# Kernel tuning notes

Hardware: AMD Instinct MI355X
Metric: run time of the kernel (lower is better)

## Reference

```python
import math
import jax, jax.numpy as jnp
import numpy as np

NSAMPLE = 16
HEADS = 4
ATTN = 256
EPS = 1e-5


def setup_inputs() -> dict:
    key = jax.random.key(0)
    ks = jax.random.split(key, 16)
    B, N, M, C = 2, 4096, 4096, 128

    def w(k, shape):
        return jax.random.normal(k, shape, jnp.float32) / np.sqrt(shape[-1]).astype(np.float32)

    return dict(
        pos1=jax.random.normal(ks[0], (B, 3, N), jnp.float32),
        pos2=jax.random.normal(ks[1], (B, 3, M), jnp.float32),
        feature1=jax.random.normal(ks[2], (B, C, N), jnp.float32),
        feature2=jax.random.normal(ks[3], (B, C, M), jnp.float32),
        w0=w(ks[4], (128, 2 * C + 3)), g0=jnp.ones(128), b0=jnp.zeros(128),
        w1=w(ks[5], (128, 128)), g1=jnp.ones(128), b1=jnp.zeros(128),
        w2=w(ks[6], (256, 128)), g2=jnp.ones(256), b2=jnp.zeros(256),
        qw=w(ks[7], (ATTN, 512)), qb=jnp.zeros(ATTN),
        kw=w(ks[8], (ATTN, C)), kb=jnp.zeros(ATTN),
        vw=w(ks[9], (ATTN, C)), vb=jnp.zeros(ATTN),
        ow=w(ks[10], (512, ATTN)), ob=jnp.zeros(512),
        lng=jnp.ones(512), lnb=jnp.zeros(512),
        fw=w(ks[11], (256, 512)), fb=jnp.zeros(256),
    )


def _knn_idx(p1t, p2t, k):
    # p1t: (B,N,3) queries; p2t: (B,M,3) keys. k nearest in pos2 for each pos1 point.
    d = (jnp.sum(p1t * p1t, -1, keepdims=True)
         - 2.0 * jnp.einsum('bnd,bmd->bnm', p1t, p2t)
         + jnp.sum(p2t * p2t, -1)[:, None, :])
    _, idx = jax.lax.top_k(-d, k)  # (B,N,k)
    return idx


def reference(pos1, pos2, feature1, feature2,
              w0, g0, b0, w1, g1, b1, w2, g2, b2,
              qw, qb, kw, kb, vw, vb, ow, ob, lng, lnb, fw, fb):
    B, _, N = pos1.shape
    M = pos2.shape[2]
    p1t = pos1.transpose(0, 2, 1)  # (B,N,3)
    p2t = pos2.transpose(0, 2, 1)  # (B,M,3)
    idx = _knn_idx(p1t, p2t, NSAMPLE)  # (B,N,k)

    gather = jax.vmap(lambda f, i: f[i])  # (M,C),(N,k)->(N,k,C)
    pos_diff = gather(p2t, idx) - p1t[:, :, None, :]              # (B,N,k,3)
    f2g = gather(feature2.transpose(0, 2, 1), idx)                # (B,N,k,C)
    f1r = jnp.broadcast_to(feature1.transpose(0, 2, 1)[:, :, None, :], f2g.shape)
    x = jnp.concatenate([pos_diff, f2g, f1r], -1)                 # (B,N,k,2C+3)

    # 1x1 conv + BatchNorm (training-mode batch stats, biased var) + ReLU
    for w, g, b in ((w0, g0, b0), (w1, g1, b1), (w2, g2, b2)):
        x = jnp.einsum('bnkc,oc->bnko', x, w)
        mu = x.mean((0, 1, 2))
        var = x.var((0, 1, 2))
        x = jax.nn.relu((x - mu) * jax.lax.rsqrt(var + EPS) * g + b)

    feat = jnp.concatenate([x.max(2), x.mean(2)], -1)  # (B,N,2*mlp[-1])

    hd = ATTN // HEADS
    f2t = feature2.transpose(0, 2, 1)  # (B,M,C)
    Q = (feat @ qw.T + qb).reshape(B, N, HEADS, hd).transpose(0, 2, 1, 3)
    K = (f2t @ kw.T + kb).reshape(B, M, HEADS, hd).transpose(0, 2, 1, 3)
    V = (f2t @ vw.T + vb).reshape(B, M, HEADS, hd).transpose(0, 2, 1, 3)
    attn = jax.nn.softmax(jnp.einsum('bhnd,bhmd->bhnm', Q, K) / math.sqrt(hd), axis=-1)
    o = jnp.einsum('bhnm,bhmd->bhnd', attn, V).transpose(0, 2, 1, 3).reshape(B, N, ATTN)
    o = o @ ow.T + ob

    y = feat + o
    mu = y.mean(-1, keepdims=True)
    var = y.var(-1, keepdims=True)
    y = (y - mu) * jax.lax.rsqrt(var + EPS) * lng + lnb
    y = y @ fw.T + fb                      # (B,N,mlp[-1])
    return (pos1, y.transpose(0, 2, 1))    # (B,3,N), (B,mlp[-1],N)
```

## Files before the change

kernel.cpp:

```cpp
#include <hip/hip_runtime.h>
#include <hip/hip_bf16.h>

constexpr int B_ = 2, N_ = 4096, M_ = 4096, C_ = 128;

typedef __attribute__((ext_vector_type(8))) __bf16 bf16x8;
typedef __attribute__((ext_vector_type(4))) float f32x4;

__global__ __launch_bounds__(256) void knn_part_kernel(const float* __restrict__ pos1,
                                                       const float* __restrict__ pos2,
                                                       float* __restrict__ pd,
                                                       int* __restrict__ pi) {
  __shared__ float tX[256], tY[256], tZ[256], tS[256];
  int tid = threadIdx.x;
  int bn = blockIdx.x * 256 + tid;
  int b = bn >> 12, n = bn & 4095;
  int seg = blockIdx.y;
  const float* p1 = pos1 + (long)b * 3 * N_;
  float qx = p1[n], qy = p1[N_ + n], qz = p1[2 * N_ + n];
  float s1 = __fadd_rn(__fadd_rn(__fmul_rn(qx, qx), __fmul_rn(qy, qy)), __fmul_rn(qz, qz));
  const float* p2 = pos2 + (long)b * 3 * M_ + seg * 256;
  {
    float x = p2[tid], y = p2[M_ + tid], z = p2[2 * M_ + tid];
    tX[tid] = x; tY[tid] = y; tZ[tid] = z;
    tS[tid] = __fadd_rn(__fadd_rn(__fmul_rn(x, x), __fmul_rn(y, y)), __fmul_rn(z, z));
  }
  __syncthreads();
  float rd[16]; int ri[16];
#pragma unroll
  for (int k = 0; k < 16; k++) { rd[k] = 3.0e38f; ri[k] = 0; }
  for (int mm = 0; mm < 256; mm += 8) {
    float dv[8];
#pragma unroll
    for (int u = 0; u < 8; u++) {
      float e = __fmaf_rn(qz, tZ[mm + u],
                          __fmaf_rn(qy, tY[mm + u], __fmul_rn(qx, tX[mm + u])));
      dv[u] = __fadd_rn(__fsub_rn(s1, __fadd_rn(e, e)), tS[mm + u]);
    }
    float thr = rd[15];
    bool any = false;
#pragma unroll
    for (int u = 0; u < 8; u++) any = any || (dv[u] < thr);
    if (any) {
#pragma unroll
      for (int u = 0; u < 8; u++) {
        float d = dv[u];
        if (d < rd[15]) {
          float cd = d; int ci = seg * 256 + mm + u;
#pragma unroll
          for (int k = 0; k < 16; k++) {
            bool lt = cd < rd[k];
            float td = lt ? rd[k] : cd;
            int ti = lt ? ri[k] : ci;
            rd[k] = lt ? cd : rd[k];
            ri[k] = lt ? ci : ri[k];
            cd = td; ci = ti;
          }
        }
      }
    }
  }
  long base = (long)seg * 16 * 8192 + bn;
#pragma unroll
  for (int k = 0; k < 16; k++) {
    pd[base + (long)k * 8192] = rd[k];
    pi[base + (long)k * 8192] = ri[k];
  }
}

__global__ __launch_bounds__(256) void knn_merge_kernel(const float* __restrict__ pd,
                                                        const int* __restrict__ pi,
                                                        int* __restrict__ idx) {
  int bn = blockIdx.x * 256 + threadIdx.x;
  float rd[16]; int ri[16];
#pragma unroll
  for (int k = 0; k < 16; k++) { rd[k] = 3.0e38f; ri[k] = 0; }
  for (int seg = 0; seg < 16; seg++) {
    for (int k = 0; k < 16; k++) {
      float d = pd[((long)seg * 16 + k) * 8192 + bn];
      if (d >= rd[15]) break;
      int ci = pi[((long)seg * 16 + k) * 8192 + bn];
      float cd = d;
#pragma unroll
      for (int j = 0; j < 16; j++) {
        bool lt = cd < rd[j];
        float td = lt ? rd[j] : cd;
        int ti = lt ? ri[j] : ci;
        rd[j] = lt ? cd : rd[j];
        ri[j] = lt ? ci : ri[j];
        cd = td; ci = ti;
      }
    }
  }
#pragma unroll
  for (int k = 0; k < 16; k++) idx[(long)bn * 16 + k] = ri[k];
}

__global__ __launch_bounds__(128) void g131_kernel(const float* __restrict__ pos,
                                                   const float* __restrict__ feat,
                                                   const float* __restrict__ w0,
                                                   float* __restrict__ out,
                                                   float sign, int woff) {
  __shared__ float Xs[131 * 16];
  int tid = threadIdx.x;
  long b = blockIdx.x >> 8;
  int i0 = (blockIdx.x & 255) * 16;
  for (int e = tid; e < 131 * 16; e += 128) {
    int r = e & 15, c = e >> 4;
    float v = (c < 3) ? sign * pos[b * 3 * N_ + (long)c * N_ + i0 + r]
                      : feat[b * C_ * N_ + (long)(c - 3) * N_ + i0 + r];
    Xs[c * 16 + r] = v;
  }
  __syncthreads();
  int o = tid;
  float acc[16];
#pragma unroll
  for (int r = 0; r < 16; r++) acc[r] = 0.f;
  for (int c = 0; c < 131; c++) {
    float wv = w0[(long)o * 259 + (c < 3 ? c : (woff + c - 3))];
    const float* xr = &Xs[c * 16];
#pragma unroll
    for (int r = 0; r < 16; r++) acc[r] = fmaf(xr[r], wv, acc[r]);
  }
#pragma unroll
  for (int r = 0; r < 16; r++) out[((b << 12) + i0 + r) * 128 + o] = acc[r];
}

__global__ __launch_bounds__(256) void z0stats_kernel(const int* __restrict__ idx,
                                                      const float* __restrict__ A1,
                                                      const float* __restrict__ A2,
                                                      double* __restrict__ st) {
  int tid = threadIdx.x;
  int o = tid & 127, half = tid >> 7;
  float sum = 0.f, sq = 0.f;
  int g0 = blockIdx.x * 32;
  for (int gi = 0; gi < 32; gi++) {
    int bn = g0 + gi;
    long b = bn >> 12;
    float a1 = A1[(long)bn * 128 + o];
    for (int k = half; k < 16; k += 2) {
      int m = idx[bn * 16 + k];
      float v = A2[(b * 4096 + m) * 128 + o] + a1;
      sum += v;
      sq += v * v;
    }
  }
  __shared__ float ls[256], lq[256];
  ls[tid] = sum; lq[tid] = sq;
  __syncthreads();
  if (tid < 128) {
    atomicAdd(&st[o], (double)(ls[tid] + ls[tid + 128]));
    atomicAdd(&st[128 + o], (double)(lq[tid] + lq[tid + 128]));
  }
}

__global__ __launch_bounds__(256) void statsb_kernel(const __hip_bfloat16* __restrict__ Z,
                                                     long nrows, double* __restrict__ st) {
  int tid = threadIdx.x;
  int c = tid & 127, sub = tid >> 7;
  long slot = (long)blockIdx.x * 2 + sub;
  long stride = (long)gridDim.x * 2;
  float sum = 0.f, sq = 0.f;
  for (long r = slot; r < nrows; r += stride) {
    float v = __bfloat162float(Z[r * 128 + c]);
    sum += v;
    sq += v * v;
  }
  __shared__ float ls[256], lq[256];
  ls[tid] = sum; lq[tid] = sq;
  __syncthreads();
  if (tid < 128) {
    atomicAdd(&st[c], (double)(ls[tid] + ls[tid + 128]));
    atomicAdd(&st[128 + c], (double)(lq[tid] + lq[tid + 128]));
  }
}

__global__ void bnfin_kernel(const double* __restrict__ st, const float* __restrict__ g,
                             const float* __restrict__ bb, float* __restrict__ sc,
                             float* __restrict__ sh, int CO, double inv) {
  int c = threadIdx.x;
  if (c < CO) {
    double mu = st[c] * inv;
    double var = st[CO + c] * inv - mu * mu;
    double rstd = 1.0 / sqrt(var + 1e-5);
    double scv = (double)g[c] * rstd;
    sc[c] = (float)scv;
    sh[c] = (float)((double)bb[c] - mu * scv);
  }
}

__global__ __launch_bounds__(256) void gemm1_mfma_kernel(
    const float* __restrict__ A2, const float* __restrict__ A1,
    const int* __restrict__ idxp, const float* __restrict__ w1,
    const float* __restrict__ sc0, const float* __restrict__ sh0,
    __hip_bfloat16* __restrict__ z1b) {
  __shared__ unsigned short As[64 * 136];
  __shared__ unsigned short Bs[64 * 136];
  __shared__ float scs[128], shs[128];
  int tid = threadIdx.x;
  int lane = tid & 63, w = tid >> 6;
  int cb = blockIdx.x;
  long r0 = (long)blockIdx.y * 64;
  int c0 = cb * 64;
  if (tid < 128) { scs[tid] = sc0[tid]; shs[tid] = sh0[tid]; }
  __syncthreads();
  {
    int row = tid >> 2, kb = (tid & 3) * 32;
    long g = r0 + row;
    int m = idxp[g];
    const float* a2p = &A2[(((g >> 16) << 12) + m) * 128 + kb];
    const float* a1p = &A1[(g >> 4) * 128 + kb];
    unsigned short* ap = &As[row * 136 + kb];
    const float* wp = &w1[(long)(c0 + row) * 128 + kb];
    unsigned short* bp = &Bs[row * 136 + kb];
#pragma unroll
    for (int h = 0; h < 4; h++) {
      union { unsigned short u[8]; uint4 v; } oa, ob;
#pragma unroll
      for (int j = 0; j < 8; j++) {
        int k = kb + h * 8 + j;
        float raw = a2p[h * 8 + j] + a1p[h * 8 + j];
        float v = fmaxf(0.f, fmaf(raw, scs[k], shs[k]));
        oa.u[j] = __bfloat16_as_ushort(__float2bfloat16(v));
        ob.u[j] = __bfloat16_as_ushort(__float2bfloat16(wp[h * 8 + j]));
      }
      *reinterpret_cast<uint4*>(ap + h * 8) = oa.v;
      *reinterpret_cast<uint4*>(bp + h * 8) = ob.v;
    }
  }
  __syncthreads();

  int fr = lane & 15, fk = (lane >> 4) * 8;
  bf16x8 a[4];
#pragma unroll
  for (int kk = 0; kk < 4; kk++)
    a[kk] = *reinterpret_cast<const bf16x8*>(&As[(w * 16 + fr) * 136 + kk * 32 + fk]);
  f32x4 acc[4];
#pragma unroll
  for (int n2 = 0; n2 < 4; n2++) {
    acc[n2] = (f32x4){0.f, 0.f, 0.f, 0.f};
#pragma unroll
    for (int kk = 0; kk < 4; kk++) {
      bf16x8 bfrag = *reinterpret_cast<const bf16x8*>(&Bs[(n2 * 16 + fr) * 136 + kk * 32 + fk]);
      acc[n2] = __builtin_amdgcn_mfma_f32_16x16x32_bf16(a[kk], bfrag, acc[n2], 0, 0, 0);
    }
  }
#pragma unroll
  for (int n2 = 0; n2 < 4; n2++) {
#pragma unroll
    for (int r = 0; r < 4; r++) {
      long row = r0 + w * 16 + (lane >> 4) * 4 + r;
      z1b[row * 128 + c0 + n2 * 16 + fr] = __float2bfloat16(acc[n2][r]);
    }
  }
}

template <int EPI>
__global__ __launch_bounds__(256) void gemm2_mfma_kernel(
    const __hip_bfloat16* __restrict__ z1b, const float* __restrict__ w2,
    const float* __restrict__ sc1, const float* __restrict__ sh1,
    const float* __restrict__ sc2, const float* __restrict__ sh2,
    float* __restrict__ feat, double* __restrict__ st) {
  __shared__ unsigned short As[64 * 136];
  __shared__ unsigned short Bs[64 * 136];
  __shared__ float scs[128], shs[128];
  __shared__ float Sred[4 * 64], Qred[4 * 64];
  int tid = threadIdx.x;
  int lane = tid & 63, w = tid >> 6;
  int cb = blockIdx.x;
  long r0 = (long)blockIdx.y * 64;
  int c0 = cb * 64;
  if (tid < 128) { scs[tid] = sc1[tid]; shs[tid] = sh1[tid]; }
  __syncthreads();
  {
    int row = tid >> 2, kb = (tid & 3) * 32;
    const __hip_bfloat16* zp = &z1b[(r0 + row) * 128 + kb];
    unsigned short* ap = &As[row * 136 + kb];
    const float* wp = &w2[(long)(c0 + row) * 128 + kb];
    unsigned short* bp = &Bs[row * 136 + kb];
#pragma unroll
    for (int h = 0; h < 4; h++) {
      union { unsigned short u[8]; uint4 v; } in, oa, ob;
      in.v = *reinterpret_cast<const uint4*>(zp + h * 8);
#pragma unroll
      for (int j = 0; j < 8; j++) {
        int k = kb + h * 8 + j;
        float f = __bfloat162float(__ushort_as_bfloat16(in.u[j]));
        float v = fmaxf(0.f, fmaf(f, scs[k], shs[k]));
        oa.u[j] = __bfloat16_as_ushort(__float2bfloat16(v));
        ob.u[j] = __bfloat16_as_ushort(__float2bfloat16(wp[h * 8 + j]));
      }
      *reinterpret_cast<uint4*>(ap + h * 8) = oa.v;
      *reinterpret_cast<uint4*>(bp + h * 8) = ob.v;
    }
  }
  __syncthreads();

  int fr = lane & 15, fk = (lane >> 4) * 8;
  bf16x8 a[4];
#pragma unroll
  for (int kk = 0; kk < 4; kk++)
    a[kk] = *reinterpret_cast<const bf16x8*>(&As[(w * 16 + fr) * 136 + kk * 32 + fk]);
  f32x4 acc[4];
#pragma unroll
  for (int n2 = 0; n2 < 4; n2++) {
    acc[n2] = (f32x4){0.f, 0.f, 0.f, 0.f};
#pragma unroll
    for (int kk = 0; kk < 4; kk++) {
      bf16x8 bfrag = *reinterpret_cast<const bf16x8*>(&Bs[(n2 * 16 + fr) * 136 + kk * 32 + fk]);
      acc[n2] = __builtin_amdgcn_mfma_f32_16x16x32_bf16(a[kk], bfrag, acc[n2], 0, 0, 0);
    }
  }

  if (EPI == 4) {
#pragma unroll
    for (int n2 = 0; n2 < 4; n2++) {
      float s = 0.f, q = 0.f;
#pragma unroll
      for (int r = 0; r < 4; r++) { s += acc[n2][r]; q += acc[n2][r] * acc[n2][r]; }
      s += __shfl_xor(s, 16); s += __shfl_xor(s, 32);
      q += __shfl_xor(q, 16); q += __shfl_xor(q, 32);
      if (lane < 16) { Sred[w * 64 + n2 * 16 + fr] = s; Qred[w * 64 + n2 * 16 + fr] = q; }
    }
    __syncthreads();
    if (tid < 64) {
      float S = Sred[tid] + Sred[64 + tid] + Sred[128 + tid] + Sred[192 + tid];
      float Q = Qred[tid] + Qred[64 + tid] + Qred[128 + tid] + Qred[192 + tid];
      atomicAdd(&st[c0 + tid], (double)S);
      atomicAdd(&st[256 + c0 + tid], (double)Q);
    }
  } else {
    int bn = (int)(r0 >> 4) + w;
#pragma unroll
    for (int n2 = 0; n2 < 4; n2++) {
      int c = c0 + n2 * 16 + fr;
      float scv = sc2[c], shv = sh2[c];
      float mx = -1e30f, sm = 0.f;
#pragma unroll
      for (int r = 0; r < 4; r++) {
        float v = fmaxf(0.f, fmaf(acc[n2][r], scv, shv));
        mx = fmaxf(mx, v);
        sm += v;
      }
      mx = fmaxf(mx, __shfl_xor(mx, 16)); mx = fmaxf(mx, __shfl_xor(mx, 32));
      sm += __shfl_xor(sm, 16); sm += __shfl_xor(sm, 32);
      if (lane < 16) {
        feat[(long)bn * 512 + c] = mx;
        feat[(long)bn * 512 + 256 + c] = sm * (1.f / 16.f);
      }
    }
  }
}

template <int EPI, int XM, bool BN>
__global__ __launch_bounds__(256) void gemm_kernel(
    const void* __restrict__ Xv, const float* __restrict__ W, float* __restrict__ out,
    int K, int CO, const float* __restrict__ bias, const float* __restrict__ sc,
    const float* __restrict__ sh, const float* __restrict__ res,
    __hip_bfloat16* __restrict__ obf, const float* __restrict__ A1,
    const int* __restrict__ idxp, double* __restrict__ st) {
  __shared__ float S[2][32 * 68];
  int tid = threadIdx.x;
  int tx = tid & 15, ty = tid >> 4;
  int cb = blockIdx.x;
  long r0 = (long)blockIdx.y * 64;
  int c0 = cb * 64;
  float acc[4][4];
#pragma unroll
  for (int i = 0; i < 4; i++)
#pragma unroll
    for (int j = 0; j < 4; j++) acc[i][j] = 0.f;

  for (int k0 = 0; k0 < K; k0 += 32) {
    if (XM != 1) {
      int c = tid & 31, rr = tid >> 5;
      float scv = 0.f, shv = 0.f;
      if (BN) { scv = sc[k0 + c]; shv = sh[k0 + c]; }
#pragma unroll
      for (int i = 0; i < 8; i++) {
        int r = rr + i * 8;
        long g = r0 + r;
        float v = ((const float*)Xv)[g * K + k0 + c];
        if (BN) v = fmaxf(0.f, fmaf(v, scv, shv));
        S[0][c * 68 + r] = v;
      }
    } else {
      int m = tid & 63, cc = tid >> 6;
      long b = r0 >> 12;
      long mg = (r0 & 4095) + m;
#pragma unroll
      for (int i = 0; i < 8; i++) {
        int c = cc + i * 4;
        S[0][c * 68 + m] = ((const float*)Xv)[(b * K + k0 + c) * 4096 + mg];
      }
    }
    {
      int c = tid & 31, oo = tid >> 5;
#pragma unroll
      for (int i = 0; i < 8; i++) {
        int o = oo + i * 8;
        S[1][c * 68 + o] = W[(long)(c0 + o) * K + k0 + c];
      }
    }
    __syncthreads();
#pragma unroll
    for (int kk = 0; kk < 32; kk++) {
      float4 a = *reinterpret_cast<const float4*>(&S[0][kk * 68 + ty * 4]);
      float4 bv = *reinterpret_cast<const float4*>(&S[1][kk * 68 + tx * 4]);
      float av[4] = {a.x, a.y, a.z, a.w};
      float bw[4] = {bv.x, bv.y, bv.z, bv.w};
#pragma unroll
      for (int i = 0; i < 4; i++)
#pragma unroll
        for (int j = 0; j < 4; j++) acc[i][j] = fmaf(av[i], bw[j], acc[i][j]);
    }
    __syncthreads();
  }

  if (EPI == 2) {
    const float4 b4 = *reinterpret_cast<const float4*>(&bias[c0 + tx * 4]);
#pragma unroll
    for (int i = 0; i < 4; i++) {
      long r = r0 + ty * 4 + i;
      float4 f4 = *reinterpret_cast<const float4*>(&res[r * CO + c0 + tx * 4]);
      float4 o4 = make_float4(acc[i][0] + b4.x + f4.x, acc[i][1] + b4.y + f4.y,
                              acc[i][2] + b4.z + f4.z, acc[i][3] + b4.w + f4.w);
      *reinterpret_cast<float4*>(&out[r * CO + c0 + tx * 4]) = o4;
    }
  } else if (EPI == 3) {
    float* Sf = &S[0][0];
#pragma unroll
    for (int j = 0; j < 4; j++) {
      float bj = bias[c0 + tx * 4 + j];
      float4 colv = make_float4(acc[0][j] + bj, acc[1][j] + bj, acc[2][j] + bj,
                                acc[3][j] + bj);
      *reinterpret_cast<float4*>(&Sf[(tx * 4 + j) * 68 + ty * 4]) = colv;
    }
    __syncthreads();
    long b = r0 >> 12;
    long n0 = (r0 & 4095);
    int n = tid & 63, oo = tid >> 6;
#pragma unroll
    for (int i = 0; i < 16; i++) {
      int o = oo + i * 4;
      out[(b * CO + c0 + o) * 4096L + n0 + n] = Sf[o * 68 + n];
    }
  } else if (EPI == 7) {
    long b = r0 >> 12;
    long nn = (r0 & 4095) + ty * 4;
    const float4 b4 = *reinterpret_cast<const float4*>(&bias[c0 + tx * 4]);
    __hip_bfloat16* Ob = obf + ((b * (CO >> 6) + cb) * 4096L) * 64;
#pragma unroll
    for (int i = 0; i < 4; i++) {
      union { unsigned short u[4]; uint2 v; } pk;
      pk.u[0] = __bfloat16_as_ushort(__float2bfloat16(acc[i][0] + b4.x));
      pk.u[1] = __bfloat16_as_ushort(__float2bfloat16(acc[i][1] + b4.y));
      pk.u[2] = __bfloat16_as_ushort(__float2bfloat16(acc[i][2] + b4.z));
      pk.u[3] = __bfloat16_as_ushort(__float2bfloat16(acc[i][3] + b4.w));
      *reinterpret_cast<uint2*>(&Ob[(nn + i) * 64 + tx * 4]) = pk.v;
    }
  } else if (EPI == 8) {
    float* Sf = &S[0][0];
#pragma unroll
    for (int j = 0; j < 4; j++) {
      float bj = bias[c0 + tx * 4 + j];
      float4 colv = make_float4(acc[0][j] + bj, acc[1][j] + bj, acc[2][j] + bj,
                                acc[3][j] + bj);
      *reinterpret_cast<float4*>(&Sf[(tx * 4 + j) * 68 + ty * 4]) = colv;
    }
    __syncthreads();
    long b = r0 >> 12;
    long n0 = (r0 & 4095);
    int n = tid & 63, oo = tid >> 6;
#pragma unroll
    for (int i = 0; i < 16; i++) {
      int o = oo + i * 4;
      obf[((b * 4 + cb) * 64 + o) * 4096L + n0 + n] = __float2bfloat16(Sf[o * 68 + n]);
    }
  }
}

__global__ __launch_bounds__(256) void flash_mfma_kernel(
    const __hip_bfloat16* __restrict__ Q, const __hip_bfloat16* __restrict__ Kb,
    const __hip_bfloat16* __restrict__ Vtg, float* __restrict__ O) {
  __shared__ unsigned short Ks[64 * 72];
  __shared__ unsigned short Vt[64 * 72];
  __shared__ unsigned short Ps[4][16 * 72];
  int tid = threadIdx.x;
  int lane = tid & 63, w = tid >> 6;
  int bh = blockIdx.x >> 6;
  int qt = blockIdx.x & 63;
  long base = (long)bh * 4096 * 64;
  int row0 = qt * 64 + w * 16;
  int fr = lane & 15;
  int fk = (lane >> 4) * 8;

  bf16x8 aq[2];
#pragma unroll
  for (int kk = 0; kk < 2; kk++)
    aq[kk] = *reinterpret_cast<const bf16x8*>(&Q[base + (long)(row0 + fr) * 64 + kk * 32 + fk]);

  f32x4 o[4];
#pragma unroll
  for (int i = 0; i < 4; i++) o[i] = (f32x4){0.f, 0.f, 0.f, 0.f};
  float m_run[4], l_run[4];
#pragma unroll
  for (int r = 0; r < 4; r++) { m_run[r] = -3.0e38f; l_run[r] = 0.f; }

  int skey = tid >> 2, sdc = (tid & 3) * 16;
  int vd = tid & 63, vkg = tid >> 6;
  int vsw = (vd ^ (vd >> 3)) & 7;

  for (int m0 = 0; m0 < 4096; m0 += 64) {
    __syncthreads();
    {
      const __hip_bfloat16* kp = &Kb[base + (long)(m0 + skey) * 64 + sdc];
      *reinterpret_cast<uint4*>(&Ks[skey * 72 + sdc]) =
          *reinterpret_cast<const uint4*>(kp);
      *reinterpret_cast<uint4*>(&Ks[skey * 72 + sdc + 8]) =
          *reinterpret_cast<const uint4*>(kp + 8);
#pragma unroll
      for (int j8 = 0; j8 < 2; j8++) {
        int k0 = vkg * 16 + j8 * 8;
        int kb = k0 >> 3;
        *reinterpret_cast<uint4*>(&Vt[vd * 72 + ((kb ^ vsw) << 3)]) =
            *reinterpret_cast<const uint4*>(&Vtg[base + (long)vd * 4096 + m0 + k0]);
      }
    }
    __syncthreads();

    f32x4 s[4];
#pragma unroll
    for (int n = 0; n < 4; n++) {
      s[n] = (f32x4){0.f, 0.f, 0.f, 0.f};
#pragma unroll
      for (int kk = 0; kk < 2; kk++) {
        bf16x8 bk = *reinterpret_cast<const bf16x8*>(&Ks[(n * 16 + fr) * 72 + kk * 32 + fk]);
        s[n] = __builtin_amdgcn_mfma_f32_16x16x32_bf16(aq[kk], bk, s[n], 0, 0, 0);
      }
    }

    float p[4][4];
#pragma unroll
    for (int r = 0; r < 4; r++) {
      float sv0 = s[0][r] * 0.125f, sv1 = s[1][r] * 0.125f;
      float sv2 = s[2][r] * 0.125f, sv3 = s[3][r] * 0.125f;
      float mx = fmaxf(fmaxf(sv0, sv1), fmaxf(sv2, sv3));
      mx = fmaxf(mx, __shfl_xor(mx, 1));
      mx = fmaxf(mx, __shfl_xor(mx, 2));
      mx = fmaxf(mx, __shfl_xor(mx, 4));
      mx = fmaxf(mx, __shfl_xor(mx, 8));
      float mn = fmaxf(m_run[r], mx);
      float fac = __expf(m_run[r] - mn);
      p[0][r] = __expf(sv0 - mn);
      p[1][r] = __expf(sv1 - mn);
      p[2][r] = __expf(sv2 - mn);
      p[3][r] = __expf(sv3 - mn);
      float rs = (p[0][r] + p[1][r]) + (p[2][r] + p[3][r]);
      rs += __shfl_xor(rs, 1);
      rs += __shfl_xor(rs, 2);
      rs += __shfl_xor(rs, 4);
      rs += __shfl_xor(rs, 8);
      l_run[r] = l_run[r] * fac + rs;
      m_run[r] = mn;
#pragma unroll
      for (int n2 = 0; n2 < 4; n2++) o[n2][r] *= fac;
    }

    unsigned short* pw = &Ps[w][0];
#pragma unroll
    for (int r = 0; r < 4; r++) {
      int prow = (lane >> 4) * 4 + r;
#pragma unroll
      for (int n = 0; n < 4; n++)
        pw[prow * 72 + n * 16 + fr] = __bfloat16_as_ushort(__float2bfloat16(p[n][r]));
    }
    bf16x8 ap[2];
#pragma unroll
    for (int kk = 0; kk < 2; kk++)
      ap[kk] = *reinterpret_cast<const bf16x8*>(&pw[fr * 72 + kk * 32 + fk]);

#pragma unroll
    for (int n2 = 0; n2 < 4; n2++) {
      int d = n2 * 16 + fr;
      int dsw = (d ^ (d >> 3)) & 7;
#pragma unroll
      for (int kk = 0; kk < 2; kk++) {
        int kb = kk * 4 + (lane >> 4);
        bf16x8 bv = *reinterpret_cast<const bf16x8*>(&Vt[d * 72 + ((kb ^ dsw) << 3)]);
        o[n2] = __builtin_amdgcn_mfma_f32_16x16x32_bf16(ap[kk], bv, o[n2], 0, 0, 0);
      }
    }
  }

  int b = bh >> 2, h = bh & 3;
#pragma unroll
  for (int r = 0; r < 4; r++) {
    float inv = 1.f / l_run[r];
    long nrow = (long)(b * 4096 + qt * 64 + w * 16 + (lane >> 4) * 4 + r);
#pragma unroll
    for (int n2 = 0; n2 < 4; n2++) {
      O[nrow * 256 + h * 64 + n2 * 16 + fr] = o[n2][r] * inv;
    }
  }
}

__global__ __launch_bounds__(256) void ln_kernel(float* __restrict__ y,
                                                 const float* __restrict__ lng,
                                                 const float* __restrict__ lnb) {
  long r = blockIdx.x;
  int tid = threadIdx.x;
  float v0 = y[r * 512 + tid];
  float v1 = y[r * 512 + 256 + tid];
  float s = v0 + v1;
  float q = v0 * v0 + v1 * v1;
#pragma unroll
  for (int off = 1; off < 64; off <<= 1) {
    s += __shfl_xor(s, off);
    q += __shfl_xor(q, off);
  }
  __shared__ float red[8];
  __shared__ float mv[2];
  int w = tid >> 6;
  if ((tid & 63) == 0) { red[w] = s; red[4 + w] = q; }
  __syncthreads();
  if (tid == 0) {
    float S = red[0] + red[1] + red[2] + red[3];
    float Q2 = red[4] + red[5] + red[6] + red[7];
    float mu = S * (1.f / 512.f);
    float var = Q2 * (1.f / 512.f) - mu * mu;
    mv[0] = mu;
    mv[1] = rsqrtf(var + 1e-5f);
  }
  __syncthreads();
  float mu = mv[0], rstd = mv[1];
  y[r * 512 + tid] = (v0 - mu) * rstd * lng[tid] + lnb[tid];
  y[r * 512 + 256 + tid] = (v1 - mu) * rstd * lng[256 + tid] + lnb[256 + tid];
}

__global__ void poscopy_kernel(const float* __restrict__ p, float* __restrict__ o) {
  int i = blockIdx.x * 256 + threadIdx.x;
  o[i] = p[i];
}

extern "C" void kernel_launch(void* const* d_in, const int* in_sizes, int n_in,
                              void* d_out, int out_size, void* d_ws, size_t ws_size,
                              hipStream_t stream) {
  (void)in_sizes; (void)n_in; (void)out_size; (void)ws_size;
  const float* pos1 = (const float*)d_in[0];
  const float* pos2 = (const float*)d_in[1];
  const float* f1 = (const float*)d_in[2];
  const float* f2 = (const float*)d_in[3];
  const float* w0 = (const float*)d_in[4];
  const float* g0 = (const float*)d_in[5];
  const float* b0 = (const float*)d_in[6];
  const float* w1 = (const float*)d_in[7];
  const float* g1 = (const float*)d_in[8];
  const float* b1 = (const float*)d_in[9];
  const float* w2 = (const float*)d_in[10];
  const float* g2 = (const float*)d_in[11];
  const float* b2 = (const float*)d_in[12];
  const float* qw = (const float*)d_in[13];
  const float* qb = (const float*)d_in[14];
  const float* kw = (const float*)d_in[15];
  const float* kb = (const float*)d_in[16];
  const float* vw = (const float*)d_in[17];
  const float* vb = (const float*)d_in[18];
  const float* ow = (const float*)d_in[19];
  const float* obv = (const float*)d_in[20];
  const float* lng = (const float*)d_in[21];
  const float* lnb = (const float*)d_in[22];
  const float* fw = (const float*)d_in[23];
  const float* fb = (const float*)d_in[24];

  char* ws = (char*)d_ws;
  __hip_bfloat16* z1b = (__hip_bfloat16*)(ws);
  __hip_bfloat16* Qbf = (__hip_bfloat16*)(ws);
  __hip_bfloat16* Kbf = (__hip_bfloat16*)(ws + (8ull << 20));
  __hip_bfloat16* Vtg = (__hip_bfloat16*)(ws + (16ull << 20));
  float* attno = (float*)(ws + (24ull << 20));
  float* y0 = (float*)(ws);
  int* idx = (int*)(ws + (32ull << 20));
  float* A1 = (float*)(ws + (33ull << 20));
  float* A2 = (float*)(ws + (37ull << 20));
  float* feat = (float*)(ws + (32ull << 20));
  char* statp = ws + (48ull << 20);
  float* pd = (float*)(ws + (56ull << 20));
  int* pi = (int*)(ws + (64ull << 20));
  double* st0 = (double*)(statp);
  double* st1 = (double*)(statp + 2048);
  double* st2 = (double*)(statp + 4096);
  float* sc0 = (float*)(statp + 8192);
  float* sh0 = (float*)(statp + 8704);
  float* sc1 = (float*)(statp + 9216);
  float* sh1 = (float*)(statp + 9728);
  float* sc2 = (float*)(statp + 10240);
  float* sh2 = (float*)(statp + 11264);

  float* out0 = (float*)d_out;
  float* out1 = out0 + 24576;

  hipMemsetAsync(statp, 0, 8192, stream);

  knn_part_kernel<<<dim3(32, 16), 256, 0, stream>>>(pos1, pos2, pd, pi);
  knn_merge_kernel<<<32, 256, 0, stream>>>(pd, pi, idx);
  g131_kernel<<<512, 128, 0, stream>>>(pos2, f2, w0, A2, 1.f, 3);
  g131_kernel<<<512, 128, 0, stream>>>(pos1, f1, w0, A1, -1.f, 131);
  z0stats_kernel<<<256, 256, 0, stream>>>(idx, A1, A2, st0);
  bnfin_kernel<<<1, 256, 0, stream>>>(st0, g0, b0, sc0, sh0, 128, 1.0 / 131072.0);
  gemm1_mfma_kernel<<<dim3(2, 2048), 256, 0, stream>>>(
      A2, A1, idx, w1, sc0, sh0, z1b);
  statsb_kernel<<<512, 256, 0, stream>>>(z1b, 131072L, st1);
  bnfin_kernel<<<1, 256, 0, stream>>>(st1, g1, b1, sc1, sh1, 128, 1.0 / 131072.0);
  gemm2_mfma_kernel<4><<<dim3(4, 2048), 256, 0, stream>>>(
      z1b, w2, sc1, sh1, nullptr, nullptr, nullptr, st2);
  bnfin_kernel<<<1, 256, 0, stream>>>(st2, g2, b2, sc2, sh2, 256, 1.0 / 131072.0);
  gemm2_mfma_kernel<5><<<dim3(4, 2048), 256, 0, stream>>>(
      z1b, w2, sc1, sh1, sc2, sh2, feat, nullptr);
  gemm_kernel<7, 0, false><<<dim3(4, 128), 256, 0, stream>>>(
      feat, qw, nullptr, 512, 256, qb, nullptr, nullptr, nullptr, Qbf, nullptr, nullptr, nullptr);
  gemm_kernel<7, 1, false><<<dim3(4, 128), 256, 0, stream>>>(
      f2, kw, nullptr, 128, 256, kb, nullptr, nullptr, nullptr, Kbf, nullptr, nullptr, nullptr);
  gemm_kernel<8, 1, false><<<dim3(4, 128), 256, 0, stream>>>(
      f2, vw, nullptr, 128, 256, vb, nullptr, nullptr, nullptr, Vtg, nullptr, nullptr, nullptr);
  flash_mfma_kernel<<<512, 256, 0, stream>>>(Qbf, Kbf, Vtg, attno);
  gemm_kernel<2, 0, false><<<dim3(8, 128), 256, 0, stream>>>(
      attno, ow, y0, 256, 512, obv, nullptr, nullptr, feat, nullptr, nullptr, nullptr, nullptr);
  ln_kernel<<<8192, 256, 0, stream>>>(y0, lng, lnb);
  gemm_kernel<3, 0, false><<<dim3(4, 128), 256, 0, stream>>>(
      y0, fw, out1, 512, 256, fb, nullptr, nullptr, nullptr, nullptr, nullptr, nullptr, nullptr);
  poscopy_kernel<<<96, 256, 0, stream>>>(pos1, out0);
}
```

Measured before the change: 804.6 us.

## Split flash attention over two key halves and merge partial softmax results

The flash attention kernel's grid gains a second dimension, and each block now handles only half of the 4096 keys. Each block writes a normalized partial output plus its running max and sum per row. A new merge kernel combines the two halves with log-sum-exp rescaling. The aim is to double the block count so more of the GPU's compute units stay busy during attention. The cost is an extra launch and about 24 MB of extra global traffic for the partial outputs.

New measurement: 792.5 us. Within noise of the previous version (-1.5%).

```diff
diff --git a/kernel.cpp b/kernel.cpp
--- a/kernel.cpp
+++ b/kernel.cpp
@@ -481,7 +481,8 @@
 
 __global__ __launch_bounds__(256) void flash_mfma_kernel(
     const __hip_bfloat16* __restrict__ Q, const __hip_bfloat16* __restrict__ Kb,
-    const __hip_bfloat16* __restrict__ Vtg, float* __restrict__ O) {
+    const __hip_bfloat16* __restrict__ Vtg, float* __restrict__ Opart,
+    float* __restrict__ mbuf, float* __restrict__ lbuf) {
   __shared__ unsigned short Ks[64 * 72];
   __shared__ unsigned short Vt[64 * 72];
   __shared__ unsigned short Ps[4][16 * 72];
@@ -489,6 +490,7 @@
   int lane = tid & 63, w = tid >> 6;
   int bh = blockIdx.x >> 6;
   int qt = blockIdx.x & 63;
+  int half = blockIdx.y;
   long base = (long)bh * 4096 * 64;
   int row0 = qt * 64 + w * 16;
   int fr = lane & 15;
@@ -510,7 +512,8 @@
   int vd = tid & 63, vkg = tid >> 6;
   int vsw = (vd ^ (vd >> 3)) & 7;
 
-  for (int m0 = 0; m0 < 4096; m0 += 64) {
+  int mstart = half * 2048;
+  for (int m0 = mstart; m0 < mstart + 2048; m0 += 64) {
     __syncthreads();
     {
       const __hip_bfloat16* kp = &Kb[base + (long)(m0 + skey) * 64 + sdc];
@@ -593,15 +596,44 @@
   }
 
   int b = bh >> 2, h = bh & 3;
+  float* Op = Opart + (long)half * 2097152;
 #pragma unroll
   for (int r = 0; r < 4; r++) {
     float inv = 1.f / l_run[r];
-    long nrow = (long)(b * 4096 + qt * 64 + w * 16 + (lane >> 4) * 4 + r);
+    int qrow = qt * 64 + w * 16 + (lane >> 4) * 4 + r;
+    long nrow = (long)(b * 4096 + qrow);
 #pragma unroll
     for (int n2 = 0; n2 < 4; n2++) {
-      O[nrow * 256 + h * 64 + n2 * 16 + fr] = o[n2][r] * inv;
-    }
-  }
+      Op[nrow * 256 + h * 64 + n2 * 16 + fr] = o[n2][r] * inv;
+    }
+    if (fr == 0) {
+      long mlrow = ((long)(half * 8 + bh)) * 4096 + qrow;
+      mbuf[mlrow] = m_run[r];
+      lbuf[mlrow] = l_run[r];
+    }
+  }
+}
+
+__global__ __launch_bounds__(256) void flash_merge_kernel(
+    const float* __restrict__ Opart, const float* __restrict__ mbuf,
+    const float* __restrict__ lbuf, float* __restrict__ O) {
+  long r = blockIdx.x;
+  int c = threadIdx.x;
+  int b = (int)(r >> 12);
+  int n = (int)(r & 4095);
+  int h = c >> 6;
+  int bh = b * 4 + h;
+  long ml0 = ((long)(0 * 8 + bh)) * 4096 + n;
+  long ml1 = ((long)(1 * 8 + bh)) * 4096 + n;
+  float m0 = mbuf[ml0], l0 = lbuf[ml0];
+  float m1 = mbuf[ml1], l1 = lbuf[ml1];
+  float M = fmaxf(m0, m1);
+  float w0 = l0 * __expf(m0 - M);
+  float w1 = l1 * __expf(m1 - M);
+  float invden = 1.f / (w0 + w1);
+  float o0 = Opart[r * 256 + c];
+  float o1 = Opart[2097152 + r * 256 + c];
+  O[r * 256 + c] = (o0 * w0 + o1 * w1) * invden;
 }
 
 __global__ __launch_bounds__(256) void ln_kernel(float* __restrict__ y,
@@ -684,8 +716,11 @@
   float* A2 = (float*)(ws + (37ull << 20));
   float* feat = (float*)(ws + (32ull << 20));
   char* statp = ws + (48ull << 20);
+  float* mbuf = (float*)(ws + (49ull << 20));
+  float* lbuf = (float*)(ws + (50ull << 20));
   float* pd = (float*)(ws + (56ull << 20));
   int* pi = (int*)(ws + (64ull << 20));
+  float* Opart = (float*)(ws + (56ull << 20));
   double* st0 = (double*)(statp);
   double* st1 = (double*)(statp + 2048);
   double* st2 = (double*)(statp + 4096);
@@ -722,7 +757,8 @@
       f2, kw, nullptr, 128, 256, kb, nullptr, nullptr, nullptr, Kbf, nullptr, nullptr, nullptr);
   gemm_kernel<8, 1, false><<<dim3(4, 128), 256, 0, stream>>>(
       f2, vw, nullptr, 128, 256, vb, nullptr, nullptr, nullptr, Vtg, nullptr, nullptr, nullptr);
-  flash_mfma_kernel<<<512, 256, 0, stream>>>(Qbf, Kbf, Vtg, attno);
+  flash_mfma_kernel<<<dim3(512, 2), 256, 0, stream>>>(Qbf, Kbf, Vtg, Opart, mbuf, lbuf);
+  flash_merge_kernel<<<8192, 256, 0, stream>>>(Opart, mbuf, lbuf, attno);
   gemm_kernel<2, 0, false><<<dim3(8, 128), 256, 0, stream>>>(
       attno, ow, y0, 256, 512, obv, nullptr, nullptr, feat, nullptr, nullptr, nullptr, nullptr);
   ln_kernel<<<8192, 256, 0, stream>>>(y0, lng, lnb);
```
